# Kernel optimization log

Hardware: AMD Instinct MI355X
Metric: run time of the kernel (lower is better)

The kernel has to match this reference:

```python
import jax, jax.numpy as jnp
import numpy as np

SINKHORN_ITERS = 100
SINKHORN_EPS = 0.1


def setup_inputs() -> dict:
    key = jax.random.key(0)
    k1, k2 = jax.random.split(key)
    M, N, C = 2048, 2048, 512
    d_M_q = jax.random.normal(k1, (M, C), dtype=jnp.float32)
    d_N_r = jax.random.normal(k2, (N, C), dtype=jnp.float32)
    # pipeline feeds L2-normalized descriptors (F.normalize(..., p=2, dim=1))
    d_M_q = d_M_q / jnp.linalg.norm(d_M_q, axis=1, keepdims=True)
    d_N_r = d_N_r / jnp.linalg.norm(d_N_r, axis=1, keepdims=True)
    z = jnp.float32(0.5)  # learned bin_score scalar
    return {"d_M_q": d_M_q, "d_N_r": d_N_r, "z": z}


def reference(d_M_q, d_N_r, z):
    M, N = d_M_q.shape[0], d_N_r.shape[0]
    # score matmul: (M, C) x (C, N) -> (M, N)
    score = jnp.einsum('mc,nc->mn', d_M_q, d_N_r)
    # augmented (M+1, N+1): dustbin row/col/corner filled with z
    S_aug = jnp.full((M + 1, N + 1), z, dtype=d_M_q.dtype).at[:M, :N].set(score)
    K0 = jnp.exp(S_aug / SINKHORN_EPS)

    def body(i, K):
        K = K / K.sum(axis=1, keepdims=True)  # row normalize
        K = K / K.sum(axis=0, keepdims=True)  # col normalize
        return K

    P_aug = jax.lax.fori_loop(0, SINKHORN_ITERS, body, K0)
    P = P_aug[:M, :N]
    return P, P_aug
```

## Files before the change

### kernel.cpp

```cpp
#include <hip/hip_runtime.h>
#include <hip/hip_fp16.h>

#define ITERS 100
#define AGENT __HIP_MEMORY_SCOPE_AGENT

union PK { unsigned long long u; struct { float v; unsigned tag; } s; };

#define SLOT 136
#define MSG_ONE (2 * 16 * 16 * SLOT)
#define UV_STRIDE 272

__device__ __forceinline__ float wave_sum(float p) {
    p += __shfl_xor(p, 1, 64);
    p += __shfl_xor(p, 2, 64);
    p += __shfl_xor(p, 4, 64);
    p += __shfl_xor(p, 8, 64);
    p += __shfl_xor(p, 16, 64);
    p += __shfl_xor(p, 32, 64);
    return p;
}

__global__ void __launch_bounds__(256, 1)
sinkhorn_fused(const float* __restrict__ Q, const float* __restrict__ R,
               const float* __restrict__ zp, float* __restrict__ out,
               unsigned long long* __restrict__ ws)
{
    __shared__ __align__(16) char smem[65536];
    float* As = (float*)smem;
    float* Bs = (float*)(smem + 32768);
    char*  TrmB = smem;
    char*  TcmB = smem + 32768;

    const int t  = threadIdx.x;
    const int b  = blockIdx.x;
    const int bi = b >> 4, bj = b & 15;
    const int tx = t & 15, ty = t >> 4;
    const int l  = t & 63, w  = t >> 6;
    const int gi0 = bi * 128, gj0 = bj * 128;

    float acc[8][8];
#pragma unroll
    for (int r = 0; r < 8; r++)
#pragma unroll
        for (int c = 0; c < 8; c++) acc[r][c] = 0.f;

    const int lr = t & 31, lc4 = t >> 5;
    const float* Qb = Q + (size_t)gi0 * 512;
    const float* Rb = R + (size_t)gj0 * 512;

    float4 qa[4], ra[4];
#pragma unroll
    for (int i = 0; i < 4; i++) {
        qa[i] = *(const float4*)(Qb + (size_t)(lr + 32 * i) * 512 + 4 * lc4);
        ra[i] = *(const float4*)(Rb + (size_t)(lr + 32 * i) * 512 + 4 * lc4);
    }
#pragma unroll
    for (int i = 0; i < 4; i++) {
        int row = lr + 32 * i;
        As[(4*lc4+0)*128 + row] = qa[i].x;  As[(4*lc4+1)*128 + row] = qa[i].y;
        As[(4*lc4+2)*128 + row] = qa[i].z;  As[(4*lc4+3)*128 + row] = qa[i].w;
        Bs[(4*lc4+0)*128 + row] = ra[i].x;  Bs[(4*lc4+1)*128 + row] = ra[i].y;
        Bs[(4*lc4+2)*128 + row] = ra[i].z;  Bs[(4*lc4+3)*128 + row] = ra[i].w;
    }
    __syncthreads();

    for (int ks = 0; ks < 16; ks++) {
        if (ks < 15) {
            int k0 = (ks + 1) * 32;
#pragma unroll
            for (int i = 0; i < 4; i++) {
                qa[i] = *(const float4*)(Qb + (size_t)(lr+32*i)*512 + k0 + 4*lc4);
                ra[i] = *(const float4*)(Rb + (size_t)(lr+32*i)*512 + k0 + 4*lc4);
            }
        }
        const float* A = As + (ks & 1) * (32 * 128);
        const float* B = Bs + (ks & 1) * (32 * 128);
#pragma unroll 4
        for (int k = 0; k < 32; k++) {
            float4 a0 = *(const float4*)(A + k*128 + 8*ty);
            float4 a1 = *(const float4*)(A + k*128 + 8*ty + 4);
            float4 b0 = *(const float4*)(B + k*128 + 8*tx);
            float4 b1 = *(const float4*)(B + k*128 + 8*tx + 4);
            float av[8] = {a0.x,a0.y,a0.z,a0.w,a1.x,a1.y,a1.z,a1.w};
            float bv[8] = {b0.x,b0.y,b0.z,b0.w,b1.x,b1.y,b1.z,b1.w};
#pragma unroll
            for (int r = 0; r < 8; r++)
#pragma unroll
                for (int c = 0; c < 8; c++)
                    acc[r][c] = fmaf(av[r], bv[c], acc[r][c]);
        }
        if (ks < 15) {
            __syncthreads();
            float* An = As + ((ks+1) & 1) * (32 * 128);
            float* Bn = Bs + ((ks+1) & 1) * (32 * 128);
#pragma unroll
            for (int i = 0; i < 4; i++) {
                int row = lr + 32 * i;
                An[(4*lc4+0)*128 + row] = qa[i].x;  An[(4*lc4+1)*128 + row] = qa[i].y;
                An[(4*lc4+2)*128 + row] = qa[i].z;  An[(4*lc4+3)*128 + row] = qa[i].w;
                Bn[(4*lc4+0)*128 + row] = ra[i].x;  Bn[(4*lc4+1)*128 + row] = ra[i].y;
                Bn[(4*lc4+2)*128 + row] = ra[i].z;  Bn[(4*lc4+3)*128 + row] = ra[i].w;
            }
            __syncthreads();
        }
    }
    __syncthreads();

    const float E = expf(zp[0] * 10.0f);
#pragma unroll
    for (int r = 0; r < 8; r++)
#pragma unroll
        for (int c = 0; c < 8; c++) acc[r][c] = expf(acc[r][c] * 10.0f);

#pragma unroll
    for (int r = 0; r < 8; r++) {
        int rr = 8 * ty + r;
        unsigned short h[8];
#pragma unroll
        for (int c = 0; c < 8; c++) h[c] = __half_as_ushort(__float2half(acc[r][c]));
        uint4 pk;
        pk.x = h[0] | ((unsigned)h[1] << 16); pk.y = h[2] | ((unsigned)h[3] << 16);
        pk.z = h[4] | ((unsigned)h[5] << 16); pk.w = h[6] | ((unsigned)h[7] << 16);
        *(uint4*)(TrmB + rr * 256 + ((tx ^ (rr & 15)) << 4)) = pk;
    }
#pragma unroll
    for (int c = 0; c < 8; c++) {
        int cc = 8 * tx + c;
        unsigned short h[8];
#pragma unroll
        for (int r = 0; r < 8; r++) h[r] = __half_as_ushort(__float2half(acc[r][c]));
        uint4 pk;
        pk.x = h[0] | ((unsigned)h[1] << 16); pk.y = h[2] | ((unsigned)h[3] << 16);
        pk.z = h[4] | ((unsigned)h[5] << 16); pk.w = h[6] | ((unsigned)h[7] << 16);
        *(uint4*)(TcmB + cc * 256 + ((ty ^ (cc & 15)) << 4)) = pk;
    }

    unsigned long long* rmsg = ws;
    unsigned long long* cmsg = ws + MSG_ONE;
    float* uvb  = (float*)(ws + 2 * MSG_ONE) + b * UV_STRIDE;
    float* ubuf = uvb;
    float* vbuf = uvb + 136;

    if (t < 128)      vbuf[t] = 1.0f;
    else if (t < 130) vbuf[t] = 64.0f;
    float uN = 0.f, vN = 1.0f, vsum = 128.0f, usum = 0.f;
    __syncthreads();

    for (int it = 0; it < ITERS; it++) {
        const int buf = it & 1;
        const unsigned tagw = (unsigned)(it + 1);

        {
            unsigned long long* base = rmsg + (size_t)((buf * 16 + bi) * 16) * SLOT;
            if (t == 128) {
                PK p; p.s.v = vsum; p.s.tag = tagw;
                __hip_atomic_store(base + (size_t)bj * SLOT + 128, p.u, __ATOMIC_RELAXED, AGENT);
            }
            if (t < 128) {
                const char* rp = TrmB + t * 256;
                const float4* v4 = (const float4*)vbuf;
                float racc = 0.f;
#pragma unroll
                for (int c = 0; c < 16; c++) {
                    uint4 kq = *(const uint4*)(rp + ((c ^ (t & 15)) << 4));
                    float4 va = v4[2 * c], vb = v4[2 * c + 1];
                    const __half2* h2 = (const __half2*)&kq;
                    float2 f;
                    f = __half22float2(h2[0]); racc = fmaf(f.x, va.x, fmaf(f.y, va.y, racc));
                    f = __half22float2(h2[1]); racc = fmaf(f.x, va.z, fmaf(f.y, va.w, racc));
                    f = __half22float2(h2[2]); racc = fmaf(f.x, vb.x, fmaf(f.y, vb.y, racc));
                    f = __half22float2(h2[3]); racc = fmaf(f.x, vb.z, fmaf(f.y, vb.w, racc));
                }
                PK p; p.s.v = racc; p.s.tag = tagw;
                __hip_atomic_store(base + (size_t)bj * SLOT + t, p.u, __ATOMIC_RELAXED, AGENT);
            }
            if (t < 128) {
                bool vdone = (l >= 16);
                float vsv = 0.f, rsum = 0.f;
                for (;;) {
                    PK m[16];
#pragma unroll
                    for (int s = 0; s < 16; s++)
                        m[s].u = __hip_atomic_load(base + (size_t)s * SLOT + t,
                                                   __ATOMIC_RELAXED, AGENT);
                    PK vm; vm.u = 0ull;
                    if (!vdone)
                        vm.u = __hip_atomic_load(base + (size_t)l * SLOT + 128,
                                                 __ATOMIC_RELAXED, AGENT);
                    int cnt = 0; float a = 0.f;
#pragma unroll
                    for (int s = 0; s < 16; s++) {
                        bool ok = (m[s].s.tag == tagw);
                        cnt += ok; a += ok ? m[s].s.v : 0.f;
                    }
                    if (!vdone && vm.s.tag == tagw) { vsv = vm.s.v; vdone = true; }
                    if (cnt == 16 && vdone) { rsum = a; break; }
                    __builtin_amdgcn_s_sleep(1);
                }
                float ssum = wave_sum(l < 16 ? vsv : 0.f);
                uN = 1.0f / (E * (ssum + vN));
                float ui = 1.0f / (rsum + E * vN);
                ubuf[t] = ui;
                float wsm = wave_sum(ui);
                if (l == 0) ubuf[128 + w] = wsm;
            }
            __syncthreads();
            usum = ubuf[128] + ubuf[129];
        }

        {
            unsigned long long* base = cmsg + (size_t)((buf * 16 + bj) * 16) * SLOT;
            if (t == 128) {
                PK p; p.s.v = usum; p.s.tag = tagw;
                __hip_atomic_store(base + (size_t)bi * SLOT + 128, p.u, __ATOMIC_RELAXED, AGENT);
            }
            if (t < 128) {
                const char* cp = TcmB + t * 256;
                const float4* u4 = (const float4*)ubuf;
                float cacc = 0.f;
#pragma unroll
                for (int c = 0; c < 16; c++) {
                    uint4 kq = *(const uint4*)(cp + ((c ^ (t & 15)) << 4));
                    float4 ua = u4[2 * c], ub = u4[2 * c + 1];
                    const __half2* h2 = (const __half2*)&kq;
                    float2 f;
                    f = __half22float2(h2[0]); cacc = fmaf(f.x, ua.x, fmaf(f.y, ua.y, cacc));
                    f = __half22float2(h2[1]); cacc = fmaf(f.x, ua.z, fmaf(f.y, ua.w, cacc));
                    f = __half22float2(h2[2]); cacc = fmaf(f.x, ub.x, fmaf(f.y, ub.y, cacc));
                    f = __half22float2(h2[3]); cacc = fmaf(f.x, ub.z, fmaf(f.y, ub.w, cacc));
                }
                PK p; p.s.v = cacc; p.s.tag = tagw;
                __hip_atomic_store(base + (size_t)bi * SLOT + t, p.u, __ATOMIC_RELAXED, AGENT);
            }
            if (t < 128) {
                bool udone = (l >= 16);
                float usv = 0.f, csum = 0.f;
                for (;;) {
                    PK m[16];
#pragma unroll
                    for (int s = 0; s < 16; s++)
                        m[s].u = __hip_atomic_load(base + (size_t)s * SLOT + t,
                                                   __ATOMIC_RELAXED, AGENT);
                    PK um; um.u = 0ull;
                    if (!udone)
                        um.u = __hip_atomic_load(base + (size_t)l * SLOT + 128,
                                                 __ATOMIC_RELAXED, AGENT);
                    int cnt = 0; float a = 0.f;
#pragma unroll
                    for (int s = 0; s < 16; s++) {
                        bool ok = (m[s].s.tag == tagw);
                        cnt += ok; a += ok ? m[s].s.v : 0.f;
                    }
                    if (!udone && um.s.tag == tagw) { usv = um.s.v; udone = true; }
                    if (cnt == 16 && udone) { csum = a; break; }
                    __builtin_amdgcn_s_sleep(1);
                }
                float ssum = wave_sum(l < 16 ? usv : 0.f);
                vN = 1.0f / (E * (ssum + uN));
                float vj = 1.0f / (csum + E * uN);
                vbuf[t] = vj;
                float wsm = wave_sum(vj);
                if (l == 0) vbuf[128 + w] = wsm;
            } else {
                bool udone = (l >= 16);
                float usv = 0.f;
                while (!udone) {
                    PK um;
                    um.u = __hip_atomic_load(base + (size_t)l * SLOT + 128,
                                             __ATOMIC_RELAXED, AGENT);
                    if (um.s.tag == tagw) { usv = um.s.v; udone = true; }
                    else __builtin_amdgcn_s_sleep(1);
                }
                float ssum = wave_sum(l < 16 ? usv : 0.f);
                vN = 1.0f / (E * (ssum + uN));
            }
            __syncthreads();
            vsum = vbuf[128] + vbuf[129];
        }
    }

    float* P  = out;
    float* PA = out + (size_t)2048 * 2048;
    float2 vv = *(const float2*)&vbuf[2 * l];
#pragma unroll 2
    for (int rr2 = 0; rr2 < 32; rr2++) {
        int i = 32 * w + rr2;
        float ui = ubuf[i];
        const char* rp = TrmB + i * 256;
        int c = l >> 2;
        __half2 h2 = *(const __half2*)(rp + ((c ^ (i & 15)) << 4) + (l & 3) * 4);
        float2 kf = __half22float2(h2);
        float p0 = ui * kf.x * vv.x;
        float p1 = ui * kf.y * vv.y;
        size_t gi = (size_t)(gi0 + i);
        *(float2*)&P[gi * 2048 + gj0 + 2 * l] = make_float2(p0, p1);
        PA[gi * 2049 + gj0 + 2 * l]     = p0;
        PA[gi * 2049 + gj0 + 2 * l + 1] = p1;
        if (bj == 15 && l == 0) PA[gi * 2049 + 2048] = ui * E * vN;
    }
    if (bi == 15 && w == 0) {
        PA[(size_t)2048 * 2049 + gj0 + 2 * l]     = uN * E * vv.x;
        PA[(size_t)2048 * 2049 + gj0 + 2 * l + 1] = uN * E * vv.y;
        if (bj == 15 && l == 0) PA[(size_t)2048 * 2049 + 2048] = uN * E * vN;
    }
}

extern "C" void kernel_launch(void* const* d_in, const int* in_sizes, int n_in,
                              void* d_out, int out_size, void* d_ws, size_t ws_size,
                              hipStream_t stream)
{
    (void)in_sizes; (void)n_in; (void)out_size; (void)ws_size;
    const float* Q  = (const float*)d_in[0];
    const float* R  = (const float*)d_in[1];
    const float* zp = (const float*)d_in[2];
    float* out = (float*)d_out;
    unsigned long long* ws = (unsigned long long*)d_ws;
    void* args[] = { (void*)&Q, (void*)&R, (void*)&zp, (void*)&out, (void*)&ws };
    hipLaunchCooperativeKernel((const void*)sinkhorn_fused, dim3(256), dim3(256),
                               args, 0, stream);
}
```

Measured before the change: 976.6 us.

## Split producer and poller waves, poll only missing slots with ballot exit

Waves 0-1 now only compute and publish the partial row/column sums. Waves 2-3, which were previously idle, poll the peer blocks' messages. The pollers track a bitmask of missing slots and re-load only those, then exit the spin loop once a wave-wide ballot shows every lane is done. The dustbin scalars uN/vN pass through LDS to the final write phase. This is meant to overlap the matvec with polling and to cut redundant atomic loads, at the cost of extra LDS handoffs and a cross-wave dependency through __syncthreads.

```diff
diff --git a/kernel.cpp b/kernel.cpp
--- a/kernel.cpp
+++ b/kernel.cpp
@@ -143,8 +143,10 @@
 
     if (t < 128)      vbuf[t] = 1.0f;
     else if (t < 130) vbuf[t] = 64.0f;
-    float uN = 0.f, vN = 1.0f, vsum = 128.0f, usum = 0.f;
+    float uN = 0.f, vN = 1.0f;
     __syncthreads();
+
+    const int pr = t - 128;
 
     for (int it = 0; it < ITERS; it++) {
         const int buf = it & 1;
@@ -152,11 +154,12 @@
 
         {
             unsigned long long* base = rmsg + (size_t)((buf * 16 + bi) * 16) * SLOT;
-            if (t == 128) {
-                PK p; p.s.v = vsum; p.s.tag = tagw;
-                __hip_atomic_store(base + (size_t)bj * SLOT + 128, p.u, __ATOMIC_RELAXED, AGENT);
-            }
             if (t < 128) {
+                if (t == 0) {
+                    PK p; p.s.v = vbuf[128] + vbuf[129]; p.s.tag = tagw;
+                    __hip_atomic_store(base + (size_t)bj * SLOT + 128, p.u,
+                                       __ATOMIC_RELAXED, AGENT);
+                }
                 const char* rp = TrmB + t * 256;
                 const float4* v4 = (const float4*)vbuf;
                 float racc = 0.f;
@@ -172,49 +175,53 @@
                     f = __half22float2(h2[3]); racc = fmaf(f.x, vb.z, fmaf(f.y, vb.w, racc));
                 }
                 PK p; p.s.v = racc; p.s.tag = tagw;
-                __hip_atomic_store(base + (size_t)bj * SLOT + t, p.u, __ATOMIC_RELAXED, AGENT);
-            }
-            if (t < 128) {
-                bool vdone = (l >= 16);
-                float vsv = 0.f, rsum = 0.f;
+                __hip_atomic_store(base + (size_t)bj * SLOT + t, p.u,
+                                   __ATOMIC_RELAXED, AGENT);
+            } else {
+                unsigned miss = 0xFFFFu;
+                bool spend = (l < 16);
+                float rsum = 0.f, ssv = 0.f;
                 for (;;) {
                     PK m[16];
 #pragma unroll
+                    for (int s = 0; s < 16; s++) {
+                        m[s].u = 0ull;
+                        if (miss & (1u << s))
+                            m[s].u = __hip_atomic_load(base + (size_t)s * SLOT + pr,
+                                                       __ATOMIC_RELAXED, AGENT);
+                    }
+                    PK sm_; sm_.u = 0ull;
+                    if (spend)
+                        sm_.u = __hip_atomic_load(base + (size_t)l * SLOT + 128,
+                                                  __ATOMIC_RELAXED, AGENT);
+#pragma unroll
                     for (int s = 0; s < 16; s++)
-                        m[s].u = __hip_atomic_load(base + (size_t)s * SLOT + t,
-                                                   __ATOMIC_RELAXED, AGENT);
-                    PK vm; vm.u = 0ull;
-                    if (!vdone)
-                        vm.u = __hip_atomic_load(base + (size_t)l * SLOT + 128,
-                                                 __ATOMIC_RELAXED, AGENT);
-                    int cnt = 0; float a = 0.f;
-#pragma unroll
-                    for (int s = 0; s < 16; s++) {
-                        bool ok = (m[s].s.tag == tagw);
-                        cnt += ok; a += ok ? m[s].s.v : 0.f;
-                    }
-                    if (!vdone && vm.s.tag == tagw) { vsv = vm.s.v; vdone = true; }
-                    if (cnt == 16 && vdone) { rsum = a; break; }
+                        if ((miss & (1u << s)) && m[s].s.tag == tagw) {
+                            rsum += m[s].s.v; miss &= ~(1u << s);
+                        }
+                    if (spend && sm_.s.tag == tagw) { ssv = sm_.s.v; spend = false; }
+                    bool done = (miss == 0) & !spend;
+                    if (__ballot(done) == ~0ull) break;
                     __builtin_amdgcn_s_sleep(1);
                 }
-                float ssum = wave_sum(l < 16 ? vsv : 0.f);
+                float ssum = wave_sum(l < 16 ? ssv : 0.f);
                 uN = 1.0f / (E * (ssum + vN));
                 float ui = 1.0f / (rsum + E * vN);
-                ubuf[t] = ui;
+                ubuf[pr] = ui;
                 float wsm = wave_sum(ui);
-                if (l == 0) ubuf[128 + w] = wsm;
+                if (l == 0) { ubuf[128 + (w - 2)] = wsm; if (w == 2) ubuf[130] = uN; }
             }
             __syncthreads();
-            usum = ubuf[128] + ubuf[129];
         }
 
         {
             unsigned long long* base = cmsg + (size_t)((buf * 16 + bj) * 16) * SLOT;
-            if (t == 128) {
-                PK p; p.s.v = usum; p.s.tag = tagw;
-                __hip_atomic_store(base + (size_t)bi * SLOT + 128, p.u, __ATOMIC_RELAXED, AGENT);
-            }
             if (t < 128) {
+                if (t == 0) {
+                    PK p; p.s.v = ubuf[128] + ubuf[129]; p.s.tag = tagw;
+                    __hip_atomic_store(base + (size_t)bi * SLOT + 128, p.u,
+                                       __ATOMIC_RELAXED, AGENT);
+                }
                 const char* cp = TcmB + t * 256;
                 const float4* u4 = (const float4*)ubuf;
                 float cacc = 0.f;
@@ -230,57 +237,50 @@
                     f = __half22float2(h2[3]); cacc = fmaf(f.x, ub.z, fmaf(f.y, ub.w, cacc));
                 }
                 PK p; p.s.v = cacc; p.s.tag = tagw;
-                __hip_atomic_store(base + (size_t)bi * SLOT + t, p.u, __ATOMIC_RELAXED, AGENT);
-            }
-            if (t < 128) {
-                bool udone = (l >= 16);
-                float usv = 0.f, csum = 0.f;
+                __hip_atomic_store(base + (size_t)bi * SLOT + t, p.u,
+                                   __ATOMIC_RELAXED, AGENT);
+            } else {
+                unsigned miss = 0xFFFFu;
+                bool spend = (l < 16);
+                float csum = 0.f, ssv = 0.f;
                 for (;;) {
                     PK m[16];
 #pragma unroll
+                    for (int s = 0; s < 16; s++) {
+                        m[s].u = 0ull;
+                        if (miss & (1u << s))
+                            m[s].u = __hip_atomic_load(base + (size_t)s * SLOT + pr,
+                                                       __ATOMIC_RELAXED, AGENT);
+                    }
+                    PK sm_; sm_.u = 0ull;
+                    if (spend)
+                        sm_.u = __hip_atomic_load(base + (size_t)l * SLOT + 128,
+                                                  __ATOMIC_RELAXED, AGENT);
+#pragma unroll
                     for (int s = 0; s < 16; s++)
-                        m[s].u = __hip_atomic_load(base + (size_t)s * SLOT + t,
-                                                   __ATOMIC_RELAXED, AGENT);
-                    PK um; um.u = 0ull;
-                    if (!udone)
-                        um.u = __hip_atomic_load(base + (size_t)l * SLOT + 128,
-                                                 __ATOMIC_RELAXED, AGENT);
-                    int cnt = 0; float a = 0.f;
-#pragma unroll
-                    for (int s = 0; s < 16; s++) {
-                        bool ok = (m[s].s.tag == tagw);
-                        cnt += ok; a += ok ? m[s].s.v : 0.f;
-                    }
-                    if (!udone && um.s.tag == tagw) { usv = um.s.v; udone = true; }
-                    if (cnt == 16 && udone) { csum = a; break; }
+                        if ((miss & (1u << s)) && m[s].s.tag == tagw) {
+                            csum += m[s].s.v; miss &= ~(1u << s);
+                        }
+                    if (spend && sm_.s.tag == tagw) { ssv = sm_.s.v; spend = false; }
+                    bool done = (miss == 0) & !spend;
+                    if (__ballot(done) == ~0ull) break;
                     __builtin_amdgcn_s_sleep(1);
                 }
-                float ssum = wave_sum(l < 16 ? usv : 0.f);
+                float ssum = wave_sum(l < 16 ? ssv : 0.f);
                 vN = 1.0f / (E * (ssum + uN));
                 float vj = 1.0f / (csum + E * uN);
-                vbuf[t] = vj;
+                vbuf[pr] = vj;
                 float wsm = wave_sum(vj);
-                if (l == 0) vbuf[128 + w] = wsm;
-            } else {
-                bool udone = (l >= 16);
-                float usv = 0.f;
-                while (!udone) {
-                    PK um;
-                    um.u = __hip_atomic_load(base + (size_t)l * SLOT + 128,
-                                             __ATOMIC_RELAXED, AGENT);
-                    if (um.s.tag == tagw) { usv = um.s.v; udone = true; }
-                    else __builtin_amdgcn_s_sleep(1);
-                }
-                float ssum = wave_sum(l < 16 ? usv : 0.f);
-                vN = 1.0f / (E * (ssum + uN));
+                if (l == 0) { vbuf[128 + (w - 2)] = wsm; if (w == 2) vbuf[130] = vN; }
             }
             __syncthreads();
-            vsum = vbuf[128] + vbuf[129];
         }
     }
 
     float* P  = out;
     float* PA = out + (size_t)2048 * 2048;
+    const float uNf = ubuf[130];
+    const float vNf = vbuf[130];
     float2 vv = *(const float2*)&vbuf[2 * l];
 #pragma unroll 2
     for (int rr2 = 0; rr2 < 32; rr2++) {
@@ -296,12 +296,12 @@
         *(float2*)&P[gi * 2048 + gj0 + 2 * l] = make_float2(p0, p1);
         PA[gi * 2049 + gj0 + 2 * l]     = p0;
         PA[gi * 2049 + gj0 + 2 * l + 1] = p1;
-        if (bj == 15 && l == 0) PA[gi * 2049 + 2048] = ui * E * vN;
+        if (bj == 15 && l == 0) PA[gi * 2049 + 2048] = ui * E * vNf;
     }
     if (bi == 15 && w == 0) {
-        PA[(size_t)2048 * 2049 + gj0 + 2 * l]     = uN * E * vv.x;
-        PA[(size_t)2048 * 2049 + gj0 + 2 * l + 1] = uN * E * vv.y;
-        if (bj == 15 && l == 0) PA[(size_t)2048 * 2049 + 2048] = uN * E * vN;
+        PA[(size_t)2048 * 2049 + gj0 + 2 * l]     = uNf * E * vv.x;
+        PA[(size_t)2048 * 2049 + gj0 + 2 * l + 1] = uNf * E * vv.y;
+        if (bj == 15 && l == 0) PA[(size_t)2048 * 2049 + 2048] = uNf * E * vNf;
     }
 }
 
```

Measured after the change: 1.456 ms. +49.0%, slower.
